# Optimization experiments

Hardware: AMD Instinct MI355X
Metric: run time of the kernel (lower is better)

Reference implementation:

```python
import jax, jax.numpy as jnp
import numpy as np

B, T = 1024, 8192


def setup_inputs() -> dict:
    key = jax.random.key(0)
    k1, k2 = jax.random.split(key)
    # phi/psi are [B, T, 2] probability-bound robustness traces in [0, 1]
    phi = jax.random.uniform(k1, (B, T, 2), dtype=jnp.float32)
    psi = jax.random.uniform(k2, (B, T, 2), dtype=jnp.float32)
    return {"phi": phi, "psi": psi}


def reference(phi, psi):
    """Until operator, interval [0, inf), exact (scale<=0) min/max.

    Original O(T^2) double loop computes, for each t:
        out[t] = max_{tau in [t, T-1]} min( min(phi[t..tau-1]), psi[tau] )
    with the empty segment (tau == t) contributing min(ones, psi[t]).
    Because min distributes over max, this satisfies the exact O(T)
    backward recurrence:
        r[t] = max( min(1, psi[t]), min(phi[t], r[t+1]) ),  r[T] = -inf
    which we evaluate with a reversed lax.scan over the time axis.
    """
    phi_t = jnp.swapaxes(phi, 0, 1)  # [T, B, 2]
    psi_t = jnp.swapaxes(psi, 0, 1)  # [T, B, 2]

    def step(carry, xs):
        p, q = xs
        v = jnp.minimum(jnp.asarray(1.0, p.dtype), q)  # tau == t term (min with ones)
        r = jnp.maximum(v, jnp.minimum(p, carry))
        return r, r

    init = jnp.full(phi_t.shape[1:], -jnp.inf, dtype=phi.dtype)  # [B, 2]
    _, out = jax.lax.scan(step, init, (phi_t, psi_t), reverse=True)
    return jnp.swapaxes(out, 0, 1)  # [B, T, 2]
```

## Files before the change

### kernel.cpp

```cpp
#include <hip/hip_runtime.h>


#define T_LEN 8192
#define K_PER 16
#define BLOCK 512

__global__ __launch_bounds__(BLOCK) void until_kernel(
    const float* __restrict__ phi, const float* __restrict__ psi,
    float* __restrict__ out)
{
    const int b   = blockIdx.x;
    const int tid = threadIdx.x;
    const size_t rowBase = (size_t)b * (T_LEN * 2);
    const float4* __restrict__ phi4 = (const float4*)(phi + rowBase);
    const float4* __restrict__ psi4 = (const float4*)(psi + rowBase);
    float4* __restrict__ out4 = (float4*)(out + rowBase);

    const float NEG = -__builtin_huge_valf();
    const float POS =  __builtin_huge_valf();

    float2 p[K_PER], v[K_PER];
#pragma unroll
    for (int j = 0; j < K_PER / 2; ++j) {
        float4 x = phi4[tid * (K_PER / 2) + j];
        p[2 * j]     = make_float2(x.x, x.y);
        p[2 * j + 1] = make_float2(x.z, x.w);
        float4 y = psi4[tid * (K_PER / 2) + j];
        v[2 * j]     = make_float2(fminf(1.0f, y.x), fminf(1.0f, y.y));
        v[2 * j + 1] = make_float2(fminf(1.0f, y.z), fminf(1.0f, y.w));
    }

    float2 A  = make_float2(NEG, NEG);
    float2 Bm = make_float2(POS, POS);
#pragma unroll
    for (int j = K_PER - 1; j >= 0; --j) {
        A.x  = fmaxf(v[j].x, fminf(p[j].x, A.x));
        A.y  = fmaxf(v[j].y, fminf(p[j].y, A.y));
        Bm.x = fminf(p[j].x, Bm.x);
        Bm.y = fminf(p[j].y, Bm.y);
    }

    __shared__ float4 sbuf[2][BLOCK];
    int cur = 0;
    sbuf[0][tid] = make_float4(A.x, A.y, Bm.x, Bm.y);
    __syncthreads();
#pragma unroll
    for (int off = 1; off < BLOCK; off <<= 1) {
        float4 f = sbuf[cur][tid];
        float4 r = f;
        if (tid + off < BLOCK) {
            float4 g = sbuf[cur][tid + off];
            r.x = fmaxf(f.x, fminf(f.z, g.x));
            r.y = fmaxf(f.y, fminf(f.w, g.y));
            r.z = fminf(f.z, g.z);
            r.w = fminf(f.w, g.w);
        }
        sbuf[cur ^ 1][tid] = r;
        cur ^= 1;
        __syncthreads();
    }

    float2 r;
    if (tid == BLOCK - 1) {
        r = make_float2(NEG, NEG);
    } else {
        float4 s = sbuf[cur][tid + 1];
        r = make_float2(s.x, s.y);
    }

    float2 hi;
#pragma unroll
    for (int j = K_PER - 1; j >= 0; --j) {
        r.x = fmaxf(v[j].x, fminf(p[j].x, r.x));
        r.y = fmaxf(v[j].y, fminf(p[j].y, r.y));
        if (j & 1) {
            hi = r;
        } else {
            out4[tid * (K_PER / 2) + (j >> 1)] =
                make_float4(r.x, r.y, hi.x, hi.y);
        }
    }
}

extern "C" void kernel_launch(void* const* d_in, const int* in_sizes, int n_in,
                              void* d_out, int out_size, void* d_ws, size_t ws_size,
                              hipStream_t stream) {
    const float* phi = (const float*)d_in[0];
    const float* psi = (const float*)d_in[1];
    float* out = (float*)d_out;
    const int Bn = in_sizes[0] / (T_LEN * 2);
    until_kernel<<<Bn, BLOCK, 0, stream>>>(phi, psi, out);
}
```

Measured before the change: 188.7 us.

## Restructure scan into per-wave shuffle scans with coalesced loads and two-pass re-read

Each wave now owns a contiguous 512-float4 segment and processes it in 8 chunks, with lanes reading consecutive float4s for coalesced access. Each chunk is scanned with a 64-lane wave shuffle. The block-level shared-memory Hillis-Steele scan and its 9 barriers are replaced by a single barrier that exchanges 8 per-wave summaries. Inputs are loaded from global memory twice, once for the summary pass and once for the output pass, instead of being held in registers. This trades extra memory traffic and shuffle work for fewer barriers and lower register pressure.

```diff
diff --git a/kernel.cpp b/kernel.cpp
--- a/kernel.cpp
+++ b/kernel.cpp
@@ -1,84 +1,106 @@
 #include <hip/hip_runtime.h>
+#include <math.h>
 
 
 #define T_LEN 8192
-#define K_PER 16
-#define BLOCK 512
+#define NSEG  8
+#define BLOCK (NSEG * 64)
+
+__device__ __forceinline__ float rfl(float x) {
+    return __int_as_float(__builtin_amdgcn_readfirstlane(__float_as_int(x)));
+}
 
 __global__ __launch_bounds__(BLOCK) void until_kernel(
     const float* __restrict__ phi, const float* __restrict__ psi,
     float* __restrict__ out)
 {
-    const int b   = blockIdx.x;
-    const int tid = threadIdx.x;
-    const size_t rowBase = (size_t)b * (T_LEN * 2);
-    const float4* __restrict__ phi4 = (const float4*)(phi + rowBase);
-    const float4* __restrict__ psi4 = (const float4*)(psi + rowBase);
-    float4* __restrict__ out4 = (float4*)(out + rowBase);
+    const int row  = blockIdx.x;
+    const int tid  = threadIdx.x;
+    const int w    = tid >> 6;
+    const int lane = tid & 63;
 
     const float NEG = -__builtin_huge_valf();
     const float POS =  __builtin_huge_valf();
 
-    float2 p[K_PER], v[K_PER];
+    const size_t segf4 = (size_t)row * (T_LEN / 2) + (size_t)w * 512;
+    const float4* __restrict__ phi4 = (const float4*)phi + segf4;
+    const float4* __restrict__ psi4 = (const float4*)psi + segf4;
+    float4* __restrict__ out4 = (float4*)out + segf4;
+
+    __shared__ float4 ssum[NSEG];
+
+    float runAx = NEG, runAy = NEG, runBx = POS, runBy = POS;
 #pragma unroll
-    for (int j = 0; j < K_PER / 2; ++j) {
-        float4 x = phi4[tid * (K_PER / 2) + j];
-        p[2 * j]     = make_float2(x.x, x.y);
-        p[2 * j + 1] = make_float2(x.z, x.w);
-        float4 y = psi4[tid * (K_PER / 2) + j];
-        v[2 * j]     = make_float2(fminf(1.0f, y.x), fminf(1.0f, y.y));
-        v[2 * j + 1] = make_float2(fminf(1.0f, y.z), fminf(1.0f, y.w));
+    for (int k = 0; k < 8; ++k) {
+        float4 P = phi4[k * 64 + lane];
+        float4 Q = psi4[k * 64 + lane];
+        float v0x = fminf(1.f, Q.x), v0y = fminf(1.f, Q.y);
+        float v1x = fminf(1.f, Q.z), v1y = fminf(1.f, Q.w);
+        float Gax = fmaxf(v0x, fminf(P.x, v1x));
+        float Gay = fmaxf(v0y, fminf(P.y, v1y));
+        float Gbx = fminf(P.x, P.z);
+        float Gby = fminf(P.y, P.w);
+#pragma unroll
+        for (int off = 1; off < 64; off <<= 1) {
+            float gax = __shfl_down(Gax, off), gay = __shfl_down(Gay, off);
+            float gbx = __shfl_down(Gbx, off), gby = __shfl_down(Gby, off);
+            bool val = (lane + off) < 64;
+            gax = val ? gax : NEG;  gay = val ? gay : NEG;
+            gbx = val ? gbx : POS;  gby = val ? gby : POS;
+            Gax = fmaxf(Gax, fminf(Gbx, gax));
+            Gay = fmaxf(Gay, fminf(Gby, gay));
+            Gbx = fminf(Gbx, gbx);
+            Gby = fminf(Gby, gby);
+        }
+        float cax = rfl(Gax), cay = rfl(Gay), cbx = rfl(Gbx), cby = rfl(Gby);
+        runAx = fmaxf(runAx, fminf(runBx, cax));
+        runAy = fmaxf(runAy, fminf(runBy, cay));
+        runBx = fminf(runBx, cbx);
+        runBy = fminf(runBy, cby);
+    }
+    if (lane == 0) ssum[w] = make_float4(runAx, runAy, runBx, runBy);
+    __syncthreads();
+
+    float rex = NEG, rey = NEG;
+    for (int j = NSEG - 1; j > w; --j) {
+        float4 s = ssum[j];
+        rex = fmaxf(s.x, fminf(s.z, rex));
+        rey = fmaxf(s.y, fminf(s.w, rey));
     }
 
-    float2 A  = make_float2(NEG, NEG);
-    float2 Bm = make_float2(POS, POS);
 #pragma unroll
-    for (int j = K_PER - 1; j >= 0; --j) {
-        A.x  = fmaxf(v[j].x, fminf(p[j].x, A.x));
-        A.y  = fmaxf(v[j].y, fminf(p[j].y, A.y));
-        Bm.x = fminf(p[j].x, Bm.x);
-        Bm.y = fminf(p[j].y, Bm.y);
-    }
-
-    __shared__ float4 sbuf[2][BLOCK];
-    int cur = 0;
-    sbuf[0][tid] = make_float4(A.x, A.y, Bm.x, Bm.y);
-    __syncthreads();
+    for (int k = 7; k >= 0; --k) {
+        float4 P = phi4[k * 64 + lane];
+        float4 Q = psi4[k * 64 + lane];
+        float v0x = fminf(1.f, Q.x), v0y = fminf(1.f, Q.y);
+        float v1x = fminf(1.f, Q.z), v1y = fminf(1.f, Q.w);
+        float Gax = fmaxf(v0x, fminf(P.x, v1x));
+        float Gay = fmaxf(v0y, fminf(P.y, v1y));
+        float Gbx = fminf(P.x, P.z);
+        float Gby = fminf(P.y, P.w);
 #pragma unroll
-    for (int off = 1; off < BLOCK; off <<= 1) {
-        float4 f = sbuf[cur][tid];
-        float4 r = f;
-        if (tid + off < BLOCK) {
-            float4 g = sbuf[cur][tid + off];
-            r.x = fmaxf(f.x, fminf(f.z, g.x));
-            r.y = fmaxf(f.y, fminf(f.w, g.y));
-            r.z = fminf(f.z, g.z);
-            r.w = fminf(f.w, g.w);
+        for (int off = 1; off < 64; off <<= 1) {
+            float gax = __shfl_down(Gax, off), gay = __shfl_down(Gay, off);
+            float gbx = __shfl_down(Gbx, off), gby = __shfl_down(Gby, off);
+            bool val = (lane + off) < 64;
+            gax = val ? gax : NEG;  gay = val ? gay : NEG;
+            gbx = val ? gbx : POS;  gby = val ? gby : POS;
+            Gax = fmaxf(Gax, fminf(Gbx, gax));
+            Gay = fmaxf(Gay, fminf(Gby, gay));
+            Gbx = fminf(Gbx, gbx);
+            Gby = fminf(Gby, gby);
         }
-        sbuf[cur ^ 1][tid] = r;
-        cur ^= 1;
-        __syncthreads();
-    }
-
-    float2 r;
-    if (tid == BLOCK - 1) {
-        r = make_float2(NEG, NEG);
-    } else {
-        float4 s = sbuf[cur][tid + 1];
-        r = make_float2(s.x, s.y);
-    }
-
-    float2 hi;
-#pragma unroll
-    for (int j = K_PER - 1; j >= 0; --j) {
-        r.x = fmaxf(v[j].x, fminf(p[j].x, r.x));
-        r.y = fmaxf(v[j].y, fminf(p[j].y, r.y));
-        if (j & 1) {
-            hi = r;
-        } else {
-            out4[tid * (K_PER / 2) + (j >> 1)] =
-                make_float4(r.x, r.y, hi.x, hi.y);
-        }
+        float yx = fmaxf(Gax, fminf(Gbx, rex));
+        float yy = fmaxf(Gay, fminf(Gby, rey));
+        float ynx = __shfl_down(yx, 1), yny = __shfl_down(yy, 1);
+        if (lane == 63) { ynx = rex; yny = rey; }
+        float r1x = fmaxf(v1x, fminf(P.z, ynx));
+        float r1y = fmaxf(v1y, fminf(P.w, yny));
+        float r0x = fmaxf(v0x, fminf(P.x, r1x));
+        float r0y = fmaxf(v0y, fminf(P.y, r1y));
+        out4[k * 64 + lane] = make_float4(r0x, r0y, r1x, r1y);
+        rex = rfl(yx);
+        rey = rfl(yy);
     }
 }
 
```

After: 186.6 us. Within noise of the previous version (-1.1%).
